# Optimization experiments

Measured on AMD Instinct MI355X. Metric: run time of the kernel, lower is better.

## Reference

```python
import jax, jax.numpy as jnp
import numpy as np

N_NODES = 100000
N_EDGES = 1000000
D_IN = 64
D_HID = 64
D_OUT = 64


def setup_inputs() -> dict:
    key = jax.random.key(0)
    ks = jax.random.split(key, 8)
    x = jax.random.normal(ks[0], (N_NODES, D_IN), dtype=jnp.float32)
    edge_index = jax.random.randint(ks[1], (2, N_EDGES), 0, N_NODES, dtype=jnp.int64)
    s = 1.0 / np.sqrt(D_IN)
    # SAGEConv layer 1: lin_l (applied to aggregated neighbors, with bias), lin_r (root, no bias)
    W1l = jax.random.uniform(ks[2], (D_HID, D_IN), jnp.float32, -s, s)
    b1l = jnp.zeros((D_HID,), jnp.float32)
    W1r = jax.random.uniform(ks[3], (D_HID, D_IN), jnp.float32, -s, s)
    s2 = 1.0 / np.sqrt(D_HID)
    W2l = jax.random.uniform(ks[4], (D_OUT, D_HID), jnp.float32, -s2, s2)
    b2l = jnp.zeros((D_OUT,), jnp.float32)
    W2r = jax.random.uniform(ks[5], (D_OUT, D_HID), jnp.float32, -s2, s2)
    return {"x": x, "edge_index": edge_index,
            "W1l": W1l, "b1l": b1l, "W1r": W1r,
            "W2l": W2l, "b2l": b2l, "W2r": W2r}


def _sage_conv(x, src, dst, Wl, bl, Wr):
    # mean-aggregate neighbor features (messages flow src -> dst)
    msg_sum = jax.ops.segment_sum(x[src], dst, num_segments=N_NODES)  # [N, d]
    deg = jax.ops.segment_sum(jnp.ones((src.shape[0],), x.dtype), dst, num_segments=N_NODES)
    agg = msg_sum / jnp.maximum(deg, 1.0)[:, None]
    return agg @ Wl.T + bl + x @ Wr.T


def reference(x, edge_index, W1l, b1l, W1r, W2l, b2l, W2r):
    src, dst = edge_index[0], edge_index[1]
    h = _sage_conv(x, src, dst, W1l, b1l, W1r)
    h = jax.nn.relu(h)
    # dropout is identity in eval mode
    out = _sage_conv(h, src, dst, W2l, b2l, W2r)
    return out
```

## Files before the change

kernel.cpp:

```cpp
#include <hip/hip_runtime.h>

#define D 64
#define BK_SHIFT 8
#define BK_MASK 255
#define SEGCAP 4096
#define ESLICE 4096

typedef __attribute__((ext_vector_type(8))) short short8;
typedef __attribute__((ext_vector_type(4))) float floatx4;

__device__ __forceinline__ ushort f2bf(float f) {
    unsigned u = __float_as_uint(f);
    u += 0x7fffu + ((u >> 16) & 1u);
    return (ushort)(u >> 16);
}
__device__ __forceinline__ float bf2f(ushort h) {
    return __int_as_float(((unsigned)h) << 16);
}

__global__ void cast_bkcount_kernel(const float* __restrict__ x, ushort* __restrict__ xh,
                                    const int* __restrict__ ei, int* __restrict__ bkcnt,
                                    int* __restrict__ scnt,
                                    int n4, int E, int B, int castb) {
    int bid = blockIdx.x;
    int tid = threadIdx.x;
    if (bid < castb) {
        int i = bid * 256 + tid;
        if (i >= n4) return;
        float4 v = ((const float4*)x)[i];
        ushort4 r;
        r.x = f2bf(v.x); r.y = f2bf(v.y); r.z = f2bf(v.z); r.w = f2bf(v.w);
        ((ushort4*)xh)[i] = r;
        return;
    }
    __shared__ int h[512];
    h[tid] = 0; h[tid + 256] = 0;
    __syncthreads();
    int slice = bid - castb;
    int e0 = slice * ESLICE;
#pragma unroll 4
    for (int it = 0; it < ESLICE / 256; ++it) {
        int e = e0 + it * 256 + tid;
        if (e < E) atomicAdd(&h[ei[E + e] >> BK_SHIFT], 1);
    }
    __syncthreads();
    scnt[slice * 512 + tid] = h[tid];
    scnt[slice * 512 + 256 + tid] = h[tid + 256];
    if (tid < B && h[tid]) atomicAdd(&bkcnt[tid], h[tid]);
    int t2 = tid + 256;
    if (t2 < B && h[t2]) atomicAdd(&bkcnt[t2], h[t2]);
}

__global__ void route_kernel(const int* __restrict__ ei, const int* __restrict__ scnt,
                             const int* __restrict__ bkcnt, int* __restrict__ bkoff,
                             int* __restrict__ bkbeg, int* __restrict__ bucketed,
                             int E, int B) {
    __shared__ int h[512];
    __shared__ int gb[512];
    __shared__ int wsum[4];
    int tid = threadIdx.x;
    int slice = blockIdx.x;
    int a = (2 * tid < B) ? bkcnt[2 * tid] : 0;
    int b = (2 * tid + 1 < B) ? bkcnt[2 * tid + 1] : 0;
    int s = a + b;
    int lane = tid & 63, w = tid >> 6;
    int p = s;
#pragma unroll
    for (int o = 1; o < 64; o <<= 1) {
        int u = __shfl_up(p, o, 64);
        if (lane >= o) p += u;
    }
    if (lane == 63) wsum[w] = p;
    __syncthreads();
    int base = 0;
    for (int ww = 0; ww < w; ++ww) base += wsum[ww];
    int excl = base + p - s;
    gb[2 * tid] = excl;
    gb[2 * tid + 1] = excl + a;
    if (slice == 0) {
        bkbeg[2 * tid] = excl;
        bkbeg[2 * tid + 1] = excl + a;
        if (tid == 255) bkbeg[512] = excl + s;
    }
    __syncthreads();
    int c0 = scnt[slice * 512 + tid];
    int c1 = scnt[slice * 512 + 256 + tid];
    if (c0) gb[tid] += atomicAdd(&bkoff[tid], c0);
    if (c1) gb[tid + 256] += atomicAdd(&bkoff[tid + 256], c1);
    h[tid] = 0; h[tid + 256] = 0;
    __syncthreads();
    int e0 = slice * ESLICE;
#pragma unroll 4
    for (int it = 0; it < ESLICE / 256; ++it) {
        int e = e0 + it * 256 + tid;
        if (e < E) {
            int dst = ei[E + e];
            int key = dst >> BK_SHIFT;
            int src = ei[e];
            int r = atomicAdd(&h[key], 1);
            bucketed[gb[key] + r] = (src << BK_SHIFT) | (dst & BK_MASK);
        }
    }
}

__global__ void csr_kernel(const int* __restrict__ bucketed, const int* __restrict__ bkbeg,
                           int* __restrict__ srclist, int* __restrict__ beg,
                           int* __restrict__ cnt, int* __restrict__ perm, int N) {
    __shared__ int lcnt[256];
    __shared__ int lbeg[256];
    __shared__ int seg[SEGCAP];
    __shared__ int wsum[4];
    __shared__ int lh[64];
    __shared__ int sfx[64];
    int k = blockIdx.x;
    int Bb = gridDim.x;
    int tid = threadIdx.x;
    int nd0 = k << BK_SHIFT;
    int nn = min(256, N - nd0);
    int L = N - (Bb - 1) * 256;
    int ebeg = bkbeg[k], eend = bkbeg[k + 1];
    int ecnt = eend - ebeg;
    lcnt[tid] = 0;
    __syncthreads();
    for (int e = ebeg + tid; e < eend; e += 256)
        atomicAdd(&lcnt[bucketed[e] & BK_MASK], 1);
    __syncthreads();
    int c = lcnt[tid];
    int lane = tid & 63, w = tid >> 6;
    int p = c;
#pragma unroll
    for (int o = 1; o < 64; o <<= 1) {
        int u = __shfl_up(p, o, 64);
        if (lane >= o) p += u;
    }
    if (lane == 63) wsum[w] = p;
    __syncthreads();
    int base = 0;
    for (int ww = 0; ww < w; ++ww) base += wsum[ww];
    int excl = base + p - c;
    lbeg[tid] = excl;
    lcnt[tid] = 0;
    __syncthreads();
    if (ecnt <= SEGCAP) {
        for (int e = ebeg + tid; e < eend; e += 256) {
            int v = bucketed[e];
            int key = v & BK_MASK;
            int pos = lbeg[key] + atomicAdd(&lcnt[key], 1);
            seg[pos] = v >> BK_SHIFT;
        }
        __syncthreads();
        for (int i = tid; i < ecnt; i += 256)
            srclist[ebeg + i] = seg[i];
    } else {
        for (int e = ebeg + tid; e < eend; e += 256) {
            int v = bucketed[e];
            int key = v & BK_MASK;
            int pos = lbeg[key] + atomicAdd(&lcnt[key], 1);
            srclist[ebeg + pos] = v >> BK_SHIFT;
        }
    }
    __syncthreads();
    int dg = 0;
    if (tid < nn) {
        dg = lcnt[tid];
        cnt[nd0 + tid] = dg;
        beg[nd0 + tid] = ebeg + lbeg[tid];
    }
    int bin = dg < 63 ? dg : 63;
    if (tid < 64) lh[tid] = 0;
    __syncthreads();
    if (tid < nn) atomicAdd(&lh[bin], 1);
    __syncthreads();
    if (tid < 64) {
        int cc = lh[tid];
        int pp = cc;
#pragma unroll
        for (int o = 1; o < 64; o <<= 1) {
            int u = __shfl_down(pp, o, 64);
            if (tid + o < 64) pp += u;
        }
        sfx[tid] = pp - cc;
        lh[tid] = 0;
    }
    __syncthreads();
    if (tid < nn) {
        int rank = sfx[bin] + atomicAdd(&lh[bin], 1);
        int pos = (rank < L) ? rank * Bb + k
                             : L * Bb + (rank - L) * (Bb - 1) + k;
        perm[pos] = nd0 + tid;
    }
}


__global__ void __launch_bounds__(256, 3) sage_kernel(
    const ushort* __restrict__ inh,
    const int* __restrict__ perm,
    const int* __restrict__ beg_, const int* __restrict__ cnt_,
    const int* __restrict__ srclist,
    const float* __restrict__ Wl, const float* __restrict__ bl,
    const float* __restrict__ Wr,
    float* __restrict__ out_f32,
    ushort* __restrict__ out_bf,
    int N, int relu) {
    __shared__ short8 fL[8][64];
    __shared__ short8 fR[8][64];
    int tid = threadIdx.x;
    int lane = tid & 63;
    {
        int c = tid >> 6;
        int n = lane & 15;
        int q = lane >> 4;
#pragma unroll
        for (int s = 0; s < 2; ++s) {
            const float* pl = Wl + (c * 16 + n) * D + s * 32 + q * 8;
            const float* pr = Wr + (c * 16 + n) * D + s * 32 + q * 8;
            short8 vl, vr;
#pragma unroll
            for (int j = 0; j < 8; ++j) {
                vl[j] = (short)f2bf(pl[j]);
                vr[j] = (short)f2bf(pr[j]);
            }
            fL[c * 2 + s][lane] = vl;
            fR[c * 2 + s][lane] = vr;
        }
    }
    __syncthreads();

    int m = lane & 15;
    int q = lane >> 4;
    float b0 = bl[m], b1 = bl[16 + m], b2 = bl[32 + m], b3 = bl[48 + m];
    int gwave   = blockIdx.x * 4 + (tid >> 6);
    int nwaves  = gridDim.x * 4;
    int ngroups = (N + 15) >> 4;

    for (int g = gwave; g < ngroups; g += nwaves) {
        int base = g * 16;
        bool nv = (base + m) < N;
        int node = nv ? perm[base + m] : 0;
        int beg = nv ? beg_[node] : 0;
        int deg = nv ? cnt_[node] : 0;

        int md = deg;
        md = max(md, __shfl_xor(md, 1, 64));
        md = max(md, __shfl_xor(md, 2, 64));
        md = max(md, __shfl_xor(md, 4, 64));
        md = max(md, __shfl_xor(md, 8, 64));

        float f0[8], f1[8];
#pragma unroll
        for (int u = 0; u < 8; ++u) { f0[u] = 0.f; f1[u] = 0.f; }

        for (int j = 0; j < md; j += 4) {
            int si0, si1, si2, si3;
            {
                int j0 = j,     i0 = beg + ((j0 < deg) ? j0 : 0);
                int j1 = j + 1, i1 = beg + ((j1 < deg) ? j1 : 0);
                int j2 = j + 2, i2 = beg + ((j2 < deg) ? j2 : 0);
                int j3 = j + 3, i3 = beg + ((j3 < deg) ? j3 : 0);
                si0 = srclist[i0]; si1 = srclist[i1];
                si2 = srclist[i2]; si3 = srclist[i3];
            }
            const ushort* rp0 = inh + (size_t)si0 * D;
            const ushort* rp1 = inh + (size_t)si1 * D;
            const ushort* rp2 = inh + (size_t)si2 * D;
            const ushort* rp3 = inh + (size_t)si3 * D;
            short8 lo0 = *(const short8*)(rp0 + q * 8);
            short8 hi0 = *(const short8*)(rp0 + 32 + q * 8);
            short8 lo1 = *(const short8*)(rp1 + q * 8);
            short8 hi1 = *(const short8*)(rp1 + 32 + q * 8);
            short8 lo2 = *(const short8*)(rp2 + q * 8);
            short8 hi2 = *(const short8*)(rp2 + 32 + q * 8);
            short8 lo3 = *(const short8*)(rp3 + q * 8);
            short8 hi3 = *(const short8*)(rp3 + 32 + q * 8);
            float m0 = (j     < deg) ? 1.f : 0.f;
            float m1 = (j + 1 < deg) ? 1.f : 0.f;
            float m2 = (j + 2 < deg) ? 1.f : 0.f;
            float m3 = (j + 3 < deg) ? 1.f : 0.f;
#pragma unroll
            for (int u = 0; u < 8; ++u) {
                f0[u] = fmaf(m0, bf2f((ushort)lo0[u]), f0[u]);
                f1[u] = fmaf(m0, bf2f((ushort)hi0[u]), f1[u]);
                f0[u] = fmaf(m1, bf2f((ushort)lo1[u]), f0[u]);
                f1[u] = fmaf(m1, bf2f((ushort)hi1[u]), f1[u]);
                f0[u] = fmaf(m2, bf2f((ushort)lo2[u]), f0[u]);
                f1[u] = fmaf(m2, bf2f((ushort)hi2[u]), f1[u]);
                f0[u] = fmaf(m3, bf2f((ushort)lo3[u]), f0[u]);
                f1[u] = fmaf(m3, bf2f((ushort)hi3[u]), f1[u]);
            }
        }

        float scale = (deg > 0) ? 1.0f / (float)deg : 0.0f;
        short8 a0, a1;
#pragma unroll
        for (int u = 0; u < 8; ++u) {
            a0[u] = (short)f2bf(f0[u] * scale);
            a1[u] = (short)f2bf(f1[u] * scale);
        }

        const ushort* rr = inh + (size_t)node * D;
        short8 r0 = *(const short8*)(rr + q * 8);
        short8 r1 = *(const short8*)(rr + 32 + q * 8);

        int on0 = __shfl(node, q * 4 + 0, 64);
        int on1 = __shfl(node, q * 4 + 1, 64);
        int on2 = __shfl(node, q * 4 + 2, 64);
        int on3 = __shfl(node, q * 4 + 3, 64);
        bool v0 = (base + q * 4 + 0) < N;
        bool v1 = (base + q * 4 + 1) < N;
        bool v2 = (base + q * 4 + 2) < N;
        bool v3 = (base + q * 4 + 3) < N;

#pragma unroll
        for (int c = 0; c < 4; ++c) {
            float bc = (c == 0) ? b0 : (c == 1) ? b1 : (c == 2) ? b2 : b3;
            floatx4 acc = {bc, bc, bc, bc};
            acc = __builtin_amdgcn_mfma_f32_16x16x32_bf16(a0, fL[c * 2 + 0][lane], acc, 0, 0, 0);
            acc = __builtin_amdgcn_mfma_f32_16x16x32_bf16(a1, fL[c * 2 + 1][lane], acc, 0, 0, 0);
            acc = __builtin_amdgcn_mfma_f32_16x16x32_bf16(r0, fR[c * 2 + 0][lane], acc, 0, 0, 0);
            acc = __builtin_amdgcn_mfma_f32_16x16x32_bf16(r1, fR[c * 2 + 1][lane], acc, 0, 0, 0);
#pragma unroll
            for (int r = 0; r < 4; ++r) {
                float v = acc[r];
                if (relu) v = fmaxf(v, 0.f);
                int onr = (r == 0) ? on0 : (r == 1) ? on1 : (r == 2) ? on2 : on3;
                bool vr = (r == 0) ? v0 : (r == 1) ? v1 : (r == 2) ? v2 : v3;
                if (vr) {
                    size_t off = (size_t)onr * D + c * 16 + m;
                    if (out_bf) out_bf[off] = f2bf(v);
                    else        out_f32[off] = v;
                }
            }
        }
    }
}

extern "C" void kernel_launch(void* const* d_in, const int* in_sizes, int n_in,
                              void* d_out, int out_size, void* d_ws, size_t ws_size,
                              hipStream_t stream) {
    const float* x   = (const float*)d_in[0];
    const int*   ei  = (const int*)d_in[1];
    const float* W1l = (const float*)d_in[2];
    const float* b1l = (const float*)d_in[3];
    const float* W1r = (const float*)d_in[4];
    const float* W2l = (const float*)d_in[5];
    const float* b2l = (const float*)d_in[6];
    const float* W2r = (const float*)d_in[7];
    float* out = (float*)d_out;

    int N = in_sizes[0] / D;
    int E = in_sizes[1] / 2;
    int B = (N + BK_MASK) >> BK_SHIFT;
    int eslices = (E + ESLICE - 1) / ESLICE;

    char* ws = (char*)d_ws;
    ushort* xh = (ushort*)ws;
    ushort* hh = xh + (size_t)N * D;
    int*   bucketed = (int*)hh;
    int*   srclist  = (int*)(ws + (size_t)2 * N * D * 2);
    int*   beg      = srclist + E + 64;
    int*   cnt      = beg + N;
    int*   perm     = cnt + N;
    int*   bkcnt    = perm + N;
    int*   bkoff    = bkcnt + 512;
    int*   bkbeg    = bkoff + 512;
    int*   scnt     = bkbeg + 513;

    (void)hipMemsetAsync(bkcnt, 0, (512 + 512) * sizeof(int), stream);

    int n4 = N * D / 4;
    int castb = (n4 + 255) / 256;
    cast_bkcount_kernel<<<castb + eslices, 256, 0, stream>>>(x, xh, ei, bkcnt, scnt,
                                                             n4, E, B, castb);
    route_kernel<<<eslices, 256, 0, stream>>>(ei, scnt, bkcnt, bkoff, bkbeg,
                                              bucketed, E, B);
    csr_kernel<<<B, 256, 0, stream>>>(bucketed, bkbeg, srclist, beg, cnt, perm, N);

    int ngroups = (N + 15) / 16;
    int sblocks = (ngroups + 3) / 4;
    sage_kernel<<<sblocks, 256, 0, stream>>>(xh, perm, beg, cnt, srclist,
                                             W1l, b1l, W1r, nullptr, hh, N, 1);
    sage_kernel<<<sblocks, 256, 0, stream>>>(hh, perm, beg, cnt, srclist,
                                             W2l, b2l, W2r, out, nullptr, N, 0);
}
```

Measured before the change: 207.7 us.

## Merge bucket count and route into one pass with fixed-capacity bucket slabs

Removes the separate count kernel, the global bucket prefix scan and the route kernel. Each edge slice now reserves space in a fixed-capacity per-bucket slab through a global atomic cursor, and edges past the capacity spill into an overflow list. The CSR kernel then rebuilds the bucket offsets from the cursors plus the overflow entries, doing the prefix scan in every block. This saves one kernel launch and one full re-read of the edge list, at the cost of a larger workspace and redundant per-block scans.

```diff
diff --git a/kernel.cpp b/kernel.cpp
--- a/kernel.cpp
+++ b/kernel.cpp
@@ -5,6 +5,7 @@
 #define BK_MASK 255
 #define SEGCAP 4096
 #define ESLICE 4096
+#define CAP 8192
 
 typedef __attribute__((ext_vector_type(8))) short short8;
 typedef __attribute__((ext_vector_type(4))) float floatx4;
@@ -18,14 +19,15 @@
     return __int_as_float(((unsigned)h) << 16);
 }
 
-__global__ void cast_bkcount_kernel(const float* __restrict__ x, ushort* __restrict__ xh,
-                                    const int* __restrict__ ei, int* __restrict__ bkcnt,
-                                    int* __restrict__ scnt,
-                                    int n4, int E, int B, int castb) {
+__global__ void cast_route_kernel(const float* __restrict__ x, ushort* __restrict__ xh,
+                                  const int* __restrict__ ei, int* __restrict__ bkcur,
+                                  int* __restrict__ ovn, int* __restrict__ ov,
+                                  int* __restrict__ bucketed2,
+                                  int n4, int E, int B, int eslices) {
     int bid = blockIdx.x;
     int tid = threadIdx.x;
-    if (bid < castb) {
-        int i = bid * 256 + tid;
+    if (bid >= eslices) {
+        int i = (bid - eslices) * 256 + tid;
         if (i >= n4) return;
         float4 v = ((const float4*)x)[i];
         ushort4 r;
@@ -34,62 +36,22 @@
         return;
     }
     __shared__ int h[512];
-    h[tid] = 0; h[tid + 256] = 0;
-    __syncthreads();
-    int slice = bid - castb;
-    int e0 = slice * ESLICE;
+    __shared__ int gb[512];
+    int t2 = tid + 256;
+    h[tid] = 0; h[t2] = 0;
+    __syncthreads();
+    int e0 = bid * ESLICE;
 #pragma unroll 4
     for (int it = 0; it < ESLICE / 256; ++it) {
         int e = e0 + it * 256 + tid;
         if (e < E) atomicAdd(&h[ei[E + e] >> BK_SHIFT], 1);
     }
     __syncthreads();
-    scnt[slice * 512 + tid] = h[tid];
-    scnt[slice * 512 + 256 + tid] = h[tid + 256];
-    if (tid < B && h[tid]) atomicAdd(&bkcnt[tid], h[tid]);
-    int t2 = tid + 256;
-    if (t2 < B && h[t2]) atomicAdd(&bkcnt[t2], h[t2]);
-}
-
-__global__ void route_kernel(const int* __restrict__ ei, const int* __restrict__ scnt,
-                             const int* __restrict__ bkcnt, int* __restrict__ bkoff,
-                             int* __restrict__ bkbeg, int* __restrict__ bucketed,
-                             int E, int B) {
-    __shared__ int h[512];
-    __shared__ int gb[512];
-    __shared__ int wsum[4];
-    int tid = threadIdx.x;
-    int slice = blockIdx.x;
-    int a = (2 * tid < B) ? bkcnt[2 * tid] : 0;
-    int b = (2 * tid + 1 < B) ? bkcnt[2 * tid + 1] : 0;
-    int s = a + b;
-    int lane = tid & 63, w = tid >> 6;
-    int p = s;
-#pragma unroll
-    for (int o = 1; o < 64; o <<= 1) {
-        int u = __shfl_up(p, o, 64);
-        if (lane >= o) p += u;
-    }
-    if (lane == 63) wsum[w] = p;
-    __syncthreads();
-    int base = 0;
-    for (int ww = 0; ww < w; ++ww) base += wsum[ww];
-    int excl = base + p - s;
-    gb[2 * tid] = excl;
-    gb[2 * tid + 1] = excl + a;
-    if (slice == 0) {
-        bkbeg[2 * tid] = excl;
-        bkbeg[2 * tid + 1] = excl + a;
-        if (tid == 255) bkbeg[512] = excl + s;
-    }
-    __syncthreads();
-    int c0 = scnt[slice * 512 + tid];
-    int c1 = scnt[slice * 512 + 256 + tid];
-    if (c0) gb[tid] += atomicAdd(&bkoff[tid], c0);
-    if (c1) gb[tid + 256] += atomicAdd(&bkoff[tid + 256], c1);
-    h[tid] = 0; h[tid + 256] = 0;
-    __syncthreads();
-    int e0 = slice * ESLICE;
+    gb[tid] = (tid < B && h[tid]) ? atomicAdd(&bkcur[tid], h[tid]) : 0;
+    gb[t2]  = (t2  < B && h[t2])  ? atomicAdd(&bkcur[t2],  h[t2])  : 0;
+    __syncthreads();
+    h[tid] = 0; h[t2] = 0;
+    __syncthreads();
 #pragma unroll 4
     for (int it = 0; it < ESLICE / 256; ++it) {
         int e = e0 + it * 256 + tid;
@@ -98,14 +60,19 @@
             int key = dst >> BK_SHIFT;
             int src = ei[e];
             int r = atomicAdd(&h[key], 1);
-            bucketed[gb[key] + r] = (src << BK_SHIFT) | (dst & BK_MASK);
-        }
-    }
-}
-
-__global__ void csr_kernel(const int* __restrict__ bucketed, const int* __restrict__ bkbeg,
+            int pos = gb[key] + r;
+            if (pos < CAP) bucketed2[(size_t)key * CAP + pos] = (src << BK_SHIFT) | (dst & BK_MASK);
+            else           ov[atomicAdd(ovn, 1)] = e;
+        }
+    }
+}
+
+__global__ void csr_kernel(const int* __restrict__ bucketed2, const int* __restrict__ ei,
+                           const int* __restrict__ bkcur, const int* __restrict__ ov,
+                           const int* __restrict__ ovn_p,
                            int* __restrict__ srclist, int* __restrict__ beg,
-                           int* __restrict__ cnt, int* __restrict__ perm, int N) {
+                           int* __restrict__ cnt, int* __restrict__ perm, int N, int E) {
+    __shared__ int btot[512];
     __shared__ int lcnt[256];
     __shared__ int lbeg[256];
     __shared__ int seg[SEGCAP];
@@ -115,19 +82,24 @@
     int k = blockIdx.x;
     int Bb = gridDim.x;
     int tid = threadIdx.x;
+    int t2 = tid + 256;
     int nd0 = k << BK_SHIFT;
     int nn = min(256, N - nd0);
     int L = N - (Bb - 1) * 256;
-    int ebeg = bkbeg[k], eend = bkbeg[k + 1];
-    int ecnt = eend - ebeg;
-    lcnt[tid] = 0;
-    __syncthreads();
-    for (int e = ebeg + tid; e < eend; e += 256)
-        atomicAdd(&lcnt[bucketed[e] & BK_MASK], 1);
-    __syncthreads();
-    int c = lcnt[tid];
+    int ovn = *ovn_p;
+    btot[tid] = (tid < Bb) ? min(bkcur[tid], CAP) : 0;
+    btot[t2]  = (t2  < Bb) ? min(bkcur[t2],  CAP) : 0;
+    __syncthreads();
+    for (int i = tid; i < ovn; i += 256)
+        atomicAdd(&btot[ei[E + ov[i]] >> BK_SHIFT], 1);
+    __syncthreads();
+    int nc   = min(bkcur[k], CAP);
+    int ecnt = btot[k];
+    int a = btot[2 * tid], b = btot[2 * tid + 1];
+    __syncthreads();
+    int s = a + b;
     int lane = tid & 63, w = tid >> 6;
-    int p = c;
+    int p = s;
 #pragma unroll
     for (int o = 1; o < 64; o <<= 1) {
         int u = __shfl_up(p, o, 64);
@@ -137,26 +109,69 @@
     __syncthreads();
     int base = 0;
     for (int ww = 0; ww < w; ++ww) base += wsum[ww];
-    int excl = base + p - c;
+    int excl = base + p - s;
+    btot[2 * tid] = excl;
+    btot[2 * tid + 1] = excl + a;
+    lcnt[tid] = 0;
+    __syncthreads();
+    int ebeg = btot[k];
+    const int* bk = bucketed2 + (size_t)k * CAP;
+    for (int i = tid; i < nc; i += 256)
+        atomicAdd(&lcnt[bk[i] & BK_MASK], 1);
+    for (int i = tid; i < ovn; i += 256) {
+        int dst = ei[E + ov[i]];
+        if ((dst >> BK_SHIFT) == k) atomicAdd(&lcnt[dst & BK_MASK], 1);
+    }
+    __syncthreads();
+    int c = lcnt[tid];
+    p = c;
+#pragma unroll
+    for (int o = 1; o < 64; o <<= 1) {
+        int u = __shfl_up(p, o, 64);
+        if (lane >= o) p += u;
+    }
+    if (lane == 63) wsum[w] = p;
+    __syncthreads();
+    base = 0;
+    for (int ww = 0; ww < w; ++ww) base += wsum[ww];
+    excl = base + p - c;
     lbeg[tid] = excl;
     lcnt[tid] = 0;
     __syncthreads();
     if (ecnt <= SEGCAP) {
-        for (int e = ebeg + tid; e < eend; e += 256) {
-            int v = bucketed[e];
+        for (int i = tid; i < nc; i += 256) {
+            int v = bk[i];
             int key = v & BK_MASK;
             int pos = lbeg[key] + atomicAdd(&lcnt[key], 1);
             seg[pos] = v >> BK_SHIFT;
+        }
+        for (int i = tid; i < ovn; i += 256) {
+            int e = ov[i];
+            int dst = ei[E + e];
+            if ((dst >> BK_SHIFT) == k) {
+                int key = dst & BK_MASK;
+                int pos = lbeg[key] + atomicAdd(&lcnt[key], 1);
+                seg[pos] = ei[e];
+            }
         }
         __syncthreads();
         for (int i = tid; i < ecnt; i += 256)
             srclist[ebeg + i] = seg[i];
     } else {
-        for (int e = ebeg + tid; e < eend; e += 256) {
-            int v = bucketed[e];
+        for (int i = tid; i < nc; i += 256) {
+            int v = bk[i];
             int key = v & BK_MASK;
             int pos = lbeg[key] + atomicAdd(&lcnt[key], 1);
             srclist[ebeg + pos] = v >> BK_SHIFT;
+        }
+        for (int i = tid; i < ovn; i += 256) {
+            int e = ov[i];
+            int dst = ei[E + e];
+            if ((dst >> BK_SHIFT) == k) {
+                int key = dst & BK_MASK;
+                int pos = lbeg[key] + atomicAdd(&lcnt[key], 1);
+                srclist[ebeg + pos] = ei[e];
+            }
         }
     }
     __syncthreads();
@@ -355,25 +370,23 @@
     char* ws = (char*)d_ws;
     ushort* xh = (ushort*)ws;
     ushort* hh = xh + (size_t)N * D;
-    int*   bucketed = (int*)hh;
     int*   srclist  = (int*)(ws + (size_t)2 * N * D * 2);
     int*   beg      = srclist + E + 64;
     int*   cnt      = beg + N;
     int*   perm     = cnt + N;
-    int*   bkcnt    = perm + N;
-    int*   bkoff    = bkcnt + 512;
-    int*   bkbeg    = bkoff + 512;
-    int*   scnt     = bkbeg + 513;
-
-    (void)hipMemsetAsync(bkcnt, 0, (512 + 512) * sizeof(int), stream);
+    int*   bkcur    = perm + N;
+    int*   ovn      = bkcur + 512;
+    int*   ov       = ovn + 4;
+    int*   bucketed2 = ov + E;
+
+    (void)hipMemsetAsync(bkcur, 0, 516 * sizeof(int), stream);
 
     int n4 = N * D / 4;
     int castb = (n4 + 255) / 256;
-    cast_bkcount_kernel<<<castb + eslices, 256, 0, stream>>>(x, xh, ei, bkcnt, scnt,
-                                                             n4, E, B, castb);
-    route_kernel<<<eslices, 256, 0, stream>>>(ei, scnt, bkcnt, bkoff, bkbeg,
-                                              bucketed, E, B);
-    csr_kernel<<<B, 256, 0, stream>>>(bucketed, bkbeg, srclist, beg, cnt, perm, N);
+    cast_route_kernel<<<eslices + castb, 256, 0, stream>>>(x, xh, ei, bkcur, ovn, ov,
+                                                           bucketed2, n4, E, B, eslices);
+    csr_kernel<<<B, 256, 0, stream>>>(bucketed2, ei, bkcur, ov, ovn,
+                                      srclist, beg, cnt, perm, N, E);
 
     int ngroups = (N + 15) / 16;
     int sblocks = (ngroups + 3) / 4;
```

Result: faster. 199.6 us (-3.9%).
